# Kernel tuning notes

Measured on AMD Instinct MI355X. Metric: run time of the kernel, lower is better.

## Reference

```python
import math
import jax, jax.numpy as jnp
import numpy as np

EMBED_DIM = 512
NUM_CLASSES = 100000
NUM_SUBCENTERS = 3
MARGIN = 0.5
SCALE = 64.0
BATCH = 256


def setup_inputs() -> dict:
    key = jax.random.key(0)
    k1, k2, k3 = jax.random.split(key, 3)
    embeddings = jax.random.normal(k1, (BATCH, EMBED_DIM), dtype=jnp.float32)
    labels = jax.random.randint(k2, (BATCH,), 0, NUM_CLASSES, dtype=jnp.int64)
    # xavier_uniform for (C*K, D): bound = sqrt(6/(fan_in+fan_out))
    fan_out, fan_in = NUM_CLASSES * NUM_SUBCENTERS, EMBED_DIM
    bound = math.sqrt(6.0 / (fan_in + fan_out))
    weight = jax.random.uniform(k3, (fan_out, fan_in), dtype=jnp.float32,
                                minval=-bound, maxval=bound)
    return {"embeddings": embeddings, "labels": labels, "weight": weight}


def reference(embeddings, labels, weight):
    eps = 1e-12
    cos_m = math.cos(MARGIN)
    sin_m = math.sin(MARGIN)
    th = math.cos(math.pi - MARGIN)
    mm = math.sin(math.pi - MARGIN) * MARGIN

    # L2 normalize (matches F.normalize with eps clamp on norm)
    e = embeddings / jnp.maximum(jnp.linalg.norm(embeddings, axis=-1, keepdims=True), eps)
    w = weight / jnp.maximum(jnp.linalg.norm(weight, axis=-1, keepdims=True), eps)

    # (N, C*K) cosine, class-major / subcenter-minor ordering like torch .view
    cosine_all = jnp.einsum('nd,md->nm', e, w).reshape(-1, NUM_CLASSES, NUM_SUBCENTERS)
    cosine = jnp.max(cosine_all, axis=2)                       # (N, C)

    sine = jnp.sqrt(jnp.clip(1.0 - jnp.square(cosine), 0.0, 1.0))
    phi = cosine * cos_m - sine * sin_m
    phi = jnp.where(cosine > th, phi, cosine - mm)

    one_hot = jax.nn.one_hot(labels, NUM_CLASSES, dtype=cosine.dtype)  # (N, C)
    logits = SCALE * (one_hot * phi + (1.0 - one_hot) * cosine)

    # mean cross entropy
    logz = jax.nn.logsumexp(logits, axis=-1)                   # (N,)
    label_logit = jnp.take_along_axis(logits, labels[:, None], axis=-1)[:, 0]
    return jnp.mean(logz - label_logit)
```

## Files before the change

### kernel.cpp

```cpp
#include <hip/hip_runtime.h>
#include <hip/hip_bf16.h>
#include <math.h>

#define EMBED_DIM 512
#define NUM_CLASSES 100000
#define NUM_SUB 3
#define BATCH 256
#define M_TOTAL (NUM_CLASSES*NUM_SUB)
#define BM 96
#define BK 64
#define LDB 72
#define NBLOCKS (M_TOTAL/BM)

typedef float  floatx4 __attribute__((ext_vector_type(4)));
typedef __bf16 bf16x8  __attribute__((ext_vector_type(8)));

__device__ __forceinline__ unsigned int f2bf(float f){
  unsigned int u = __float_as_uint(f);
  u += 0x7FFFu + ((u >> 16) & 1u);
  return u >> 16;
}

__device__ __forceinline__ void gload_lds16(const void* g, void* l){
  __builtin_amdgcn_global_load_lds(
      (const __attribute__((address_space(1))) unsigned int*)g,
      (__attribute__((address_space(3))) unsigned int*)l,
      16, 0, 0);
}

__global__ __launch_bounds__(64) void normalize_pack(
    const float* __restrict__ E, unsigned short* __restrict__ ehat)
{
  const int r    = blockIdx.x;
  const int lane = threadIdx.x;
  const float4 v0 = *(const float4*)(E + r*EMBED_DIM + lane*8);
  const float4 v1 = *(const float4*)(E + r*EMBED_DIM + lane*8 + 4);
  float ssq = v0.x*v0.x + v0.y*v0.y + v0.z*v0.z + v0.w*v0.w
            + v1.x*v1.x + v1.y*v1.y + v1.z*v1.z + v1.w*v1.w;
  #pragma unroll
  for (int m = 1; m < 64; m <<= 1) ssq += __shfl_xor(ssq, m, 64);
  float nn = sqrtf(ssq);
  nn = fmaxf(nn, 1e-12f);
  const float rn = 1.0f / nn;
  const float vals[8] = {v0.x, v0.y, v0.z, v0.w, v1.x, v1.y, v1.z, v1.w};
  unsigned int p[4];
  #pragma unroll
  for (int i = 0; i < 4; ++i)
    p[i] = f2bf(vals[2*i]*rn) | (f2bf(vals[2*i+1]*rn) << 16);
  const int kt = lane >> 3;
  const size_t off = (size_t)kt*(BATCH*BK) + (size_t)r*BK + (lane & 7)*8;
  *(uint4*)(ehat + off) = make_uint4(p[0], p[1], p[2], p[3]);
}

__global__ __launch_bounds__(256, 2) void arcface_main(
    const float* __restrict__ W,
    const unsigned short* __restrict__ ehat,
    const int* __restrict__ labels,
    float* __restrict__ gsum,
    float* __restrict__ llogit)
{
  __shared__ char  smem[50176];
  __shared__ float snorm[BM];

  const int tid  = threadIdx.x;
  const int wave = tid >> 6, lane = tid & 63;
  const int m0   = blockIdx.x * BM;

  unsigned short* lA = (unsigned short*)smem;
  unsigned short* lB = (unsigned short*)(smem + 32768);

  floatx4 acc[24] = {};
  float ssq_acc[6] = {0,0,0,0,0,0};
  const int r16 = tid >> 4, c4 = tid & 15;

  for (int kt = 0; kt < 8; ++kt){
    {
      const char* asrc = (const char*)ehat + kt*32768 + wave*8192 + lane*16;
      char*       adst = smem + wave*8192 + lane*16;
      #pragma unroll
      for (int i = 0; i < 8; ++i) gload_lds16(asrc + i*1024, adst + i*1024);
    }
    #pragma unroll
    for (int it = 0; it < 6; ++it){
      const int row = it*16 + r16;
      const float4 v = *(const float4*)(W + (size_t)(m0 + row)*EMBED_DIM + kt*BK + c4*4);
      ssq_acc[it] += v.x*v.x + v.y*v.y + v.z*v.z + v.w*v.w;
      const unsigned int p0 = f2bf(v.x) | (f2bf(v.y) << 16);
      const unsigned int p1 = f2bf(v.z) | (f2bf(v.w) << 16);
      *(uint2*)(lB + row*LDB + c4*4) = make_uint2(p0, p1);
    }
    __syncthreads();
    #pragma unroll
    for (int h = 0; h < 2; ++h){
      bf16x8 a[4], b[6];
      #pragma unroll
      for (int rt = 0; rt < 4; ++rt)
        a[rt] = *(const bf16x8*)(lA + (wave*64 + rt*16 + (lane & 15))*64 + h*32 + (lane >> 4)*8);
      #pragma unroll
      for (int ct = 0; ct < 6; ++ct)
        b[ct] = *(const bf16x8*)(lB + (ct*16 + (lane & 15))*LDB + h*32 + (lane >> 4)*8);
      #pragma unroll
      for (int rt = 0; rt < 4; ++rt)
        #pragma unroll
        for (int ct = 0; ct < 6; ++ct)
          acc[rt*6 + ct] = __builtin_amdgcn_mfma_f32_16x16x32_bf16(
              a[rt], b[ct], acc[rt*6 + ct], 0, 0, 0);
    }
    __syncthreads();
  }

  #pragma unroll
  for (int it = 0; it < 6; ++it){
    float s = ssq_acc[it];
    s += __shfl_xor(s, 1, 64); s += __shfl_xor(s, 2, 64);
    s += __shfl_xor(s, 4, 64); s += __shfl_xor(s, 8, 64);
    if (c4 == 0) snorm[it*16 + r16] = s;
  }
  __syncthreads();

  const int col = lane & 15, quad = lane >> 4;
  float rnorm6[6];
  #pragma unroll
  for (int i = 0; i < 6; ++i){
    float nw = sqrtf(snorm[i*16 + col]);
    rnorm6[i] = 1.0f / fmaxf(nw, 1e-12f);
  }
  const int   nrow = wave*64 + lane;
  const int   lbl  = labels[nrow];
  float*      ebuf = (float*)smem + wave*(64*49);
  float       contrib = 0.0f;
  const float cos_m = 0.87758256189037276f;
  const float sin_m = 0.47942553860420301f;
  const float thr   = -0.87758256189037276f;
  const float mmv   = 0.23971276930210156f;
  const int   cls0  = m0 / 3;

  #pragma unroll
  for (int half = 0; half < 2; ++half){
    #pragma unroll
    for (int ct = 0; ct < 3; ++ct){
      const int ctg = half*3 + ct;
      #pragma unroll
      for (int rt = 0; rt < 4; ++rt)
        #pragma unroll
        for (int r = 0; r < 4; ++r)
          ebuf[(rt*16 + quad*4 + r)*49 + ct*16 + col] = acc[rt*6 + ctg][r] * rnorm6[ctg];
    }
    __syncthreads();
    for (int c = 0; c < 16; ++c){
      const float a0 = ebuf[lane*49 + 3*c + 0];
      const float a1 = ebuf[lane*49 + 3*c + 1];
      const float a2 = ebuf[lane*49 + 3*c + 2];
      float cm = fmaxf(a0, fmaxf(a1, a2));
      float val = cm;
      const int cls = cls0 + half*16 + c;
      if (cls == lbl){
        const float sine = sqrtf(fmaxf(0.0f, 1.0f - cm*cm));
        const float phi  = cm*cos_m - sine*sin_m;
        val = (cm > thr) ? phi : (cm - mmv);
        llogit[nrow] = 64.0f * val;
      }
      contrib += __expf(64.0f*val - 64.0f);
    }
    __syncthreads();
  }
  atomicAdd(&gsum[nrow*16], contrib);
}

__global__ __launch_bounds__(256) void finalize_loss(
    const float* __restrict__ gsum, const float* __restrict__ llogit,
    float* __restrict__ out)
{
  const int tid = threadIdx.x;
  float v = logf(gsum[tid*16]) + 64.0f - llogit[tid];
  #pragma unroll
  for (int m = 1; m < 64; m <<= 1) v += __shfl_xor(v, m, 64);
  __shared__ float red[4];
  if ((tid & 63) == 0) red[tid >> 6] = v;
  __syncthreads();
  if (tid == 0) out[0] = (red[0] + red[1] + red[2] + red[3]) * (1.0f/BATCH);
}

extern "C" void kernel_launch(void* const* d_in, const int* in_sizes, int n_in,
                              void* d_out, int out_size, void* d_ws, size_t ws_size,
                              hipStream_t stream)
{
  const float* emb    = (const float*)d_in[0];
  const int*   labels = (const int*)d_in[1];
  const float* W      = (const float*)d_in[2];

  unsigned short* ehat   = (unsigned short*)d_ws;
  float*          gsum   = (float*)((char*)d_ws + 262144);
  float*          llogit = (float*)((char*)d_ws + 262144 + 16384);

  hipMemsetAsync(gsum, 0, 16384, stream);
  normalize_pack<<<BATCH, 64, 0, stream>>>(emb, ehat);
  arcface_main<<<NBLOCKS, 256, 0, stream>>>(W, ehat, labels, gsum, llogit);
  finalize_loss<<<1, 256, 0, stream>>>(gsum, llogit, (float*)d_out);
}
```

Measured before the change: 842.2 us.

## Double-buffer W tiles in LDS and load A fragments directly to registers

After: 947.4 us. 1.13x slower.

```diff
diff --git a/kernel.cpp b/kernel.cpp
--- a/kernel.cpp
+++ b/kernel.cpp
@@ -21,13 +21,6 @@
   return u >> 16;
 }
 
-__device__ __forceinline__ void gload_lds16(const void* g, void* l){
-  __builtin_amdgcn_global_load_lds(
-      (const __attribute__((address_space(1))) unsigned int*)g,
-      (__attribute__((address_space(3))) unsigned int*)l,
-      16, 0, 0);
-}
-
 __global__ __launch_bounds__(64) void normalize_pack(
     const float* __restrict__ E, unsigned short* __restrict__ ehat)
 {
@@ -65,46 +58,79 @@
   const int tid  = threadIdx.x;
   const int wave = tid >> 6, lane = tid & 63;
   const int m0   = blockIdx.x * BM;
-
-  unsigned short* lA = (unsigned short*)smem;
-  unsigned short* lB = (unsigned short*)(smem + 32768);
+  const int r16  = tid >> 4, c4 = tid & 15;
+  const int col  = lane & 15, quad = lane >> 4;
 
   floatx4 acc[24] = {};
   float ssq_acc[6] = {0,0,0,0,0,0};
-  const int r16 = tid >> 4, c4 = tid & 15;
-
-  for (int kt = 0; kt < 8; ++kt){
-    {
-      const char* asrc = (const char*)ehat + kt*32768 + wave*8192 + lane*16;
-      char*       adst = smem + wave*8192 + lane*16;
-      #pragma unroll
-      for (int i = 0; i < 8; ++i) gload_lds16(asrc + i*1024, adst + i*1024);
-    }
+
+  const unsigned short* abase = ehat + (wave*64 + col)*64 + quad*8;
+  const float* wbase = W + (size_t)m0*EMBED_DIM + c4*4;
+
+  bf16x8 areg[2][4][2];
+  float4 bv[6];
+
+  #pragma unroll
+  for (int it = 0; it < 6; ++it)
+    bv[it] = *(const float4*)(wbase + (size_t)(it*16 + r16)*EMBED_DIM);
+  #pragma unroll
+  for (int rt = 0; rt < 4; ++rt)
+    #pragma unroll
+    for (int h = 0; h < 2; ++h)
+      areg[0][rt][h] = *(const bf16x8*)(abase + rt*1024 + h*32);
+  {
+    unsigned short* lBw = (unsigned short*)smem;
     #pragma unroll
     for (int it = 0; it < 6; ++it){
       const int row = it*16 + r16;
-      const float4 v = *(const float4*)(W + (size_t)(m0 + row)*EMBED_DIM + kt*BK + c4*4);
+      const float4 v = bv[it];
       ssq_acc[it] += v.x*v.x + v.y*v.y + v.z*v.z + v.w*v.w;
-      const unsigned int p0 = f2bf(v.x) | (f2bf(v.y) << 16);
-      const unsigned int p1 = f2bf(v.z) | (f2bf(v.w) << 16);
-      *(uint2*)(lB + row*LDB + c4*4) = make_uint2(p0, p1);
-    }
-    __syncthreads();
+      *(uint2*)(lBw + row*LDB + c4*4) =
+          make_uint2(f2bf(v.x) | (f2bf(v.y) << 16), f2bf(v.z) | (f2bf(v.w) << 16));
+    }
+  }
+  __syncthreads();
+
+  #pragma unroll
+  for (int kt = 0; kt < 8; ++kt){
+    const int cur = kt & 1, nxt = cur ^ 1;
+    unsigned short* lBr = (unsigned short*)(smem + cur*13824);
+    unsigned short* lBw = (unsigned short*)(smem + nxt*13824);
+
+    if (kt < 7){
+      #pragma unroll
+      for (int it = 0; it < 6; ++it)
+        bv[it] = *(const float4*)(wbase + (size_t)(it*16 + r16)*EMBED_DIM + (kt+1)*BK);
+      #pragma unroll
+      for (int rt = 0; rt < 4; ++rt)
+        #pragma unroll
+        for (int h = 0; h < 2; ++h)
+          areg[nxt][rt][h] = *(const bf16x8*)(abase + (kt+1)*16384 + rt*1024 + h*32);
+    }
+
     #pragma unroll
     for (int h = 0; h < 2; ++h){
-      bf16x8 a[4], b[6];
-      #pragma unroll
-      for (int rt = 0; rt < 4; ++rt)
-        a[rt] = *(const bf16x8*)(lA + (wave*64 + rt*16 + (lane & 15))*64 + h*32 + (lane >> 4)*8);
+      bf16x8 b[6];
       #pragma unroll
       for (int ct = 0; ct < 6; ++ct)
-        b[ct] = *(const bf16x8*)(lB + (ct*16 + (lane & 15))*LDB + h*32 + (lane >> 4)*8);
+        b[ct] = *(const bf16x8*)(lBr + (ct*16 + col)*LDB + h*32 + quad*8);
       #pragma unroll
       for (int rt = 0; rt < 4; ++rt)
         #pragma unroll
         for (int ct = 0; ct < 6; ++ct)
           acc[rt*6 + ct] = __builtin_amdgcn_mfma_f32_16x16x32_bf16(
-              a[rt], b[ct], acc[rt*6 + ct], 0, 0, 0);
+              areg[cur][rt][h], b[ct], acc[rt*6 + ct], 0, 0, 0);
+    }
+
+    if (kt < 7){
+      #pragma unroll
+      for (int it = 0; it < 6; ++it){
+        const int row = it*16 + r16;
+        const float4 v = bv[it];
+        ssq_acc[it] += v.x*v.x + v.y*v.y + v.z*v.z + v.w*v.w;
+        *(uint2*)(lBw + row*LDB + c4*4) =
+            make_uint2(f2bf(v.x) | (f2bf(v.y) << 16), f2bf(v.z) | (f2bf(v.w) << 16));
+      }
     }
     __syncthreads();
   }
@@ -118,7 +144,6 @@
   }
   __syncthreads();
 
-  const int col = lane & 15, quad = lane >> 4;
   float rnorm6[6];
   #pragma unroll
   for (int i = 0; i < 6; ++i){
```
